# Optimization experiments

Measured on AMD Instinct MI355X. Metric: run time of the kernel, lower is better.

Reference implementation:

```python
import jax, jax.numpy as jnp
import numpy as np

CAPACITY = 1024


def setup_inputs() -> dict:
    T, H, I, E, K = 2048, 1024, 1408, 8, 2
    key = jax.random.key(0)
    k0, k1, k2, k3, k4 = jax.random.split(key, 5)
    hidden_states = jax.random.normal(k0, (T, H), dtype=jnp.float32)
    w1 = jax.random.normal(k1, (E, 2 * I, H), dtype=jnp.float32) * 0.02  # [gate; up]
    w2 = jax.random.normal(k2, (E, H, I), dtype=jnp.float32) * 0.02
    topk_weights = jax.random.uniform(k3, (T, K), dtype=jnp.float32)
    topk_ids = jax.random.randint(k4, (T, K), 0, E, dtype=jnp.int32)
    return {"hidden_states": hidden_states, "w1": w1, "w2": w2,
            "topk_weights": topk_weights, "topk_ids": topk_ids}


def reference(hidden_states, w1, w2, topk_weights, topk_ids):
    # MoE: prepare(dispatch) -> grouped expert GEMM (silu-gated MLP) -> finalize(combine)
    T, H = hidden_states.shape
    E = w1.shape[0]
    I = w2.shape[2]
    K = topk_ids.shape[1]
    C = CAPACITY

    # ---- prepare: dispatch token copies to per-expert buffers ----
    flat_ids = topk_ids.reshape(-1)                       # (T*K,)
    onehot = jax.nn.one_hot(flat_ids, E, dtype=jnp.int32)  # (T*K, E)
    cs = jnp.cumsum(onehot, axis=0)                        # running per-expert counts
    pos = jnp.take_along_axis(cs, flat_ids[:, None], axis=1)[:, 0] - 1  # slot in expert buffer
    keep = pos < C
    pos_c = jnp.where(keep, pos, 0)

    x_flat = jnp.repeat(hidden_states, K, axis=0)          # (T*K, H)
    x_e = jnp.zeros((E, C, H), dtype=hidden_states.dtype)
    x_e = x_e.at[flat_ids, pos_c].add(jnp.where(keep[:, None], x_flat, 0.0))

    # ---- grouped expert GEMM: silu(gate) * up, then down-proj ----
    h = jnp.einsum('ech,eoh->eco', x_e, w1)                # (E, C, 2I)
    gate, up = h[..., :I], h[..., I:]
    act = jax.nn.silu(gate) * up                           # (E, C, I)
    y = jnp.einsum('eci,ehi->ech', act, w2)                # (E, C, H)

    # ---- finalize: gather back, apply router weights, reduce over top-k ----
    y_flat = y[flat_ids, pos_c] * (keep[:, None].astype(y.dtype)) \
             * topk_weights.reshape(-1, 1)                 # (T*K, H)
    out = y_flat.reshape(T, K, H).sum(axis=1)              # (T, H)
    return out.astype(hidden_states.dtype)
```

## Files before the change

kernel.cpp:

```cpp
#include <hip/hip_runtime.h>

#define NE 8
#define CAP 1024
#define HD 1024
#define ID 1408
#define TT 2048

typedef __attribute__((ext_vector_type(8))) short bf16x8;
typedef __attribute__((ext_vector_type(4))) float f32x4;
typedef unsigned short u16;
typedef unsigned int u32;
typedef unsigned long long u64;

__device__ __forceinline__ u16 f2bf(float f) {
  u32 u = __float_as_uint(f);
  u = (u + 0x7fffu + ((u >> 16) & 1u)) >> 16;
  return (u16)u;
}

__device__ __forceinline__ void async_cp16(const void* g, void* l) {
  __builtin_amdgcn_global_load_lds(
      (const __attribute__((address_space(1))) u32*)g,
      (__attribute__((address_space(3))) u32*)l, 16, 0, 0);
}

#define W1_BLKS (2 * ID * NE)
#define W2_BLKS (NE * HD * ID / 4 / 256)
#define X_BLKS (TT * HD / 4 / 256)
__global__ void prep_kernel(const float4* __restrict__ w1, ushort4* __restrict__ bw1,
                            const float4* __restrict__ w2, ushort4* __restrict__ bw2,
                            const float4* __restrict__ x, ushort4* __restrict__ bx,
                            float4* __restrict__ out) {
  int b = blockIdx.x;
  int tid = threadIdx.x;
  if (b < W1_BLKS) {
    int n = b % (2 * ID);
    int e = b / (2 * ID);
    int j = (n < ID) ? n : (n - ID);
    int np = (j >> 4) * 32 + (j & 15) + ((n < ID) ? 0 : 16);
    float4 v = w1[((size_t)e * 2 * ID + n) * (HD / 4) + tid];
    ushort4 o;
    o.x = f2bf(v.x); o.y = f2bf(v.y); o.z = f2bf(v.z); o.w = f2bf(v.w);
    bw1[((size_t)e * 2 * ID + np) * (HD / 4) + tid] = o;
  } else if (b < W1_BLKS + W2_BLKS) {
    size_t i = (size_t)(b - W1_BLKS) * 256 + tid;
    float4 v = w2[i];
    ushort4 o;
    o.x = f2bf(v.x); o.y = f2bf(v.y); o.z = f2bf(v.z); o.w = f2bf(v.w);
    bw2[i] = o;
  } else {
    size_t i = (size_t)(b - W1_BLKS - W2_BLKS) * 256 + tid;
    float4 v = x[i];
    ushort4 o;
    o.x = f2bf(v.x); o.y = f2bf(v.y); o.z = f2bf(v.z); o.w = f2bf(v.w);
    bx[i] = o;
    out[i] = float4{0.f, 0.f, 0.f, 0.f};
  }
}

__global__ void route_kernel(const int* __restrict__ ids, int* __restrict__ rowmap,
                             int* __restrict__ flatpos, int* __restrict__ counts) {
  __shared__ int ids_s[TT * 2];
  __shared__ int sc[256][NE + 1];
  int tid = threadIdx.x;
  for (int i = tid; i < TT * 2; i += 256) ids_s[i] = ids[i];
  __syncthreads();
  int base = tid * 16;
  u64 own64 = 0;
#pragma unroll
  for (int j = 0; j < 16; ++j) own64 += 1ull << (ids_s[base + j] * 8);
  int own[NE];
#pragma unroll
  for (int e = 0; e < NE; ++e) { own[e] = (int)((own64 >> (e * 8)) & 0xff); sc[tid][e] = own[e]; }
  __syncthreads();
  for (int off = 1; off < 256; off <<= 1) {
    int v[NE];
    if (tid >= off) {
#pragma unroll
      for (int e = 0; e < NE; ++e) v[e] = sc[tid - off][e];
    }
    __syncthreads();
    if (tid >= off) {
#pragma unroll
      for (int e = 0; e < NE; ++e) sc[tid][e] += v[e];
    }
    __syncthreads();
  }
  if (tid == 255) {
#pragma unroll
    for (int e = 0; e < NE; ++e) counts[e] = sc[255][e] < CAP ? sc[255][e] : CAP;
  }
  int excl[NE];
#pragma unroll
  for (int e = 0; e < NE; ++e) excl[e] = sc[tid][e] - own[e];
  __syncthreads();
#pragma unroll
  for (int e = 0; e < NE; ++e) sc[tid][e] = excl[e];
#pragma unroll
  for (int j = 0; j < 16; ++j) {
    int f = base + j;
    int e = ids_s[f];
    int p = sc[tid][e]++;
    if (p < CAP) { rowmap[e * CAP + p] = f; flatpos[f] = p; }
    else flatpos[f] = -1;
  }
}

__global__ __launch_bounds__(256) void gemm1_kernel(
    const u16* __restrict__ A, const u16* __restrict__ B, u16* __restrict__ Hb,
    const int* __restrict__ rowmap, const int* __restrict__ counts) {
  int e = blockIdx.x;
  int count = counts[e];
  int m0 = blockIdx.y * 64;
  if (m0 >= count) return;
  int n0 = blockIdx.z * 128;
  int tid = threadIdx.x;
  int lane = tid & 63, wid = tid >> 6;
  int wm = wid >> 1, wn = wid & 1;
  int q = lane >> 4, lm = lane & 15;

  __shared__ __align__(16) char smA[64 * 128];
  __shared__ __align__(16) char smB[128 * 128];

  int rloc = tid >> 3;
  int chs = ((tid & 7) ^ (rloc & 7)) * 8;
  const u16* aP[2];
  const u16* bP[4];
#pragma unroll
  for (int i = 0; i < 2; ++i) {
    int gr = m0 + rloc + 32 * i;
    int f = (gr < count) ? rowmap[e * CAP + gr] : 0;
    aP[i] = A + (size_t)(f >> 1) * HD + chs;
  }
#pragma unroll
  for (int i = 0; i < 4; ++i)
    bP[i] = B + ((size_t)e * 2 * ID + n0 + rloc + 32 * i) * HD + chs;

  f32x4 zero = {0.f, 0.f, 0.f, 0.f};
  f32x4 acc[2][4];
#pragma unroll
  for (int mi = 0; mi < 2; ++mi)
#pragma unroll
    for (int ni = 0; ni < 4; ++ni) acc[mi][ni] = zero;

  for (int kt = 0; kt < HD / 64; ++kt) {
    int ko = kt * 64;
#pragma unroll
    for (int i = 0; i < 2; ++i)
      async_cp16(aP[i] + ko, smA + (i * 256 + tid) * 16);
#pragma unroll
    for (int i = 0; i < 4; ++i)
      async_cp16(bP[i] + ko, smB + (i * 256 + tid) * 16);
    asm volatile("s_waitcnt vmcnt(0)" ::: "memory");
    __syncthreads();
#pragma unroll
    for (int s = 0; s < 2; ++s) {
      bf16x8 af[2], bfr[4];
#pragma unroll
      for (int mi = 0; mi < 2; ++mi) {
        int row = wm * 32 + mi * 16 + lm;
        af[mi] = *(const bf16x8*)(smA + row * 128 + (((s * 4 + q) ^ (lm & 7)) * 16));
      }
#pragma unroll
      for (int ni = 0; ni < 4; ++ni) {
        int row = wn * 64 + ni * 16 + lm;
        bfr[ni] = *(const bf16x8*)(smB + row * 128 + (((s * 4 + q) ^ (lm & 7)) * 16));
      }
#pragma unroll
      for (int mi = 0; mi < 2; ++mi)
#pragma unroll
        for (int ni = 0; ni < 4; ++ni)
          acc[mi][ni] = __builtin_amdgcn_mfma_f32_16x16x32_bf16(af[mi], bfr[ni], acc[mi][ni], 0, 0, 0);
    }
    __syncthreads();
  }

  u16* smOut = (u16*)smB;
#pragma unroll
  for (int mi = 0; mi < 2; ++mi) {
#pragma unroll
    for (int k = 0; k < 2; ++k) {
      int colL = wn * 32 + k * 16 + lm;
#pragma unroll
      for (int r = 0; r < 4; ++r) {
        float g = acc[mi][2 * k][r];
        float u = acc[mi][2 * k + 1][r];
        float a = g / (1.f + __expf(-g)) * u;
        int row = wm * 32 + mi * 16 + q * 4 + r;
        smOut[row * 72 + colL] = f2bf(a);
      }
    }
  }
  __syncthreads();
  {
    int row = tid >> 2, seg = tid & 3;
    const u16* sp = smOut + row * 72 + seg * 16;
    bf16x8 v0 = *(const bf16x8*)sp;
    bf16x8 v1 = *(const bf16x8*)(sp + 8);
    u16* dp = Hb + ((size_t)e * CAP + m0 + row) * ID + (n0 >> 1) + seg * 16;
    *(bf16x8*)dp = v0;
    *(bf16x8*)(dp + 8) = v1;
  }
}

__global__ __launch_bounds__(256) void gemm2_kernel(
    const u16* __restrict__ A, const u16* __restrict__ B, float* __restrict__ out,
    const int* __restrict__ rowmap, const int* __restrict__ counts,
    const float* __restrict__ tw) {
  int e = blockIdx.x;
  int count = counts[e];
  int m0 = blockIdx.y * 64;
  if (m0 >= count) return;
  int n0 = blockIdx.z * 64;
  int tid = threadIdx.x;
  int lane = tid & 63, wid = tid >> 6;
  int wm = wid >> 1, wn = wid & 1;
  int q = lane >> 4, lm = lane & 15;

  __shared__ __align__(16) char smA[64 * 128];
  __shared__ __align__(16) char smB[64 * 128];

  int rloc = tid >> 3;
  int chs = ((tid & 7) ^ (rloc & 7)) * 8;
  const u16* aP[2];
  const u16* bP[2];
#pragma unroll
  for (int i = 0; i < 2; ++i) {
    aP[i] = A + ((size_t)e * CAP + m0 + rloc + 32 * i) * ID + chs;
    bP[i] = B + ((size_t)e * HD + n0 + rloc + 32 * i) * ID + chs;
  }

  f32x4 zero = {0.f, 0.f, 0.f, 0.f};
  f32x4 acc[2][2];
#pragma unroll
  for (int mi = 0; mi < 2; ++mi)
#pragma unroll
    for (int ni = 0; ni < 2; ++ni) acc[mi][ni] = zero;

  for (int kt = 0; kt < ID / 64; ++kt) {
    int ko = kt * 64;
#pragma unroll
    for (int i = 0; i < 2; ++i) {
      async_cp16(aP[i] + ko, smA + (i * 256 + tid) * 16);
      async_cp16(bP[i] + ko, smB + (i * 256 + tid) * 16);
    }
    asm volatile("s_waitcnt vmcnt(0)" ::: "memory");
    __syncthreads();
#pragma unroll
    for (int s = 0; s < 2; ++s) {
      bf16x8 af[2], bfr[2];
#pragma unroll
      for (int mi = 0; mi < 2; ++mi) {
        int row = wm * 32 + mi * 16 + lm;
        af[mi] = *(const bf16x8*)(smA + row * 128 + (((s * 4 + q) ^ (lm & 7)) * 16));
      }
#pragma unroll
      for (int ni = 0; ni < 2; ++ni) {
        int row = wn * 32 + ni * 16 + lm;
        bfr[ni] = *(const bf16x8*)(smB + row * 128 + (((s * 4 + q) ^ (lm & 7)) * 16));
      }
#pragma unroll
      for (int mi = 0; mi < 2; ++mi)
#pragma unroll
        for (int ni = 0; ni < 2; ++ni)
          acc[mi][ni] = __builtin_amdgcn_mfma_f32_16x16x32_bf16(af[mi], bfr[ni], acc[mi][ni], 0, 0, 0);
    }
    __syncthreads();
  }

#pragma unroll
  for (int mi = 0; mi < 2; ++mi) {
#pragma unroll
    for (int r = 0; r < 4; ++r) {
      int grow = m0 + wm * 32 + mi * 16 + q * 4 + r;
      if (grow < count) {
        int f = rowmap[e * CAP + grow];
        float w = tw[f];
        int t = f >> 1;
#pragma unroll
        for (int ni = 0; ni < 2; ++ni) {
          int col = n0 + wn * 32 + ni * 16 + lm;
          atomicAdd(&out[(size_t)t * HD + col], w * acc[mi][ni][r]);
        }
      }
    }
  }
}

extern "C" void kernel_launch(void* const* d_in, const int* in_sizes, int n_in,
                              void* d_out, int out_size, void* d_ws, size_t ws_size,
                              hipStream_t stream) {
  const float* hidden = (const float*)d_in[0];
  const float* w1 = (const float*)d_in[1];
  const float* w2 = (const float*)d_in[2];
  const float* tw = (const float*)d_in[3];
  const int* ids = (const int*)d_in[4];
  float* out = (float*)d_out;

  char* p = (char*)d_ws;
  auto alloc = [&](size_t b) { char* r = p; p += (b + 255) & ~(size_t)255; return r; };
  u16* bw1 = (u16*)alloc((size_t)NE * 2 * ID * HD * 2);
  u16* bw2 = (u16*)alloc((size_t)NE * HD * ID * 2);
  u16* bx = (u16*)alloc((size_t)TT * HD * 2);
  u16* hbuf = (u16*)alloc((size_t)NE * CAP * ID * 2);
  int* rowmap = (int*)alloc((size_t)NE * CAP * 4);
  int* flatpos = (int*)alloc((size_t)TT * 2 * 4);
  int* counts = (int*)alloc((size_t)NE * 4);

  prep_kernel<<<W1_BLKS + W2_BLKS + X_BLKS, 256, 0, stream>>>(
      (const float4*)w1, (ushort4*)bw1, (const float4*)w2, (ushort4*)bw2,
      (const float4*)hidden, (ushort4*)bx, (float4*)out);

  route_kernel<<<1, 256, 0, stream>>>(ids, rowmap, flatpos, counts);

  gemm1_kernel<<<dim3(NE, CAP / 64, 2 * ID / 128), 256, 0, stream>>>(
      bx, bw1, hbuf, rowmap, counts);

  gemm2_kernel<<<dim3(NE, CAP / 64, HD / 64), 256, 0, stream>>>(
      hbuf, bw2, out, rowmap, counts, tw);
}
```

Measured before the change: 265.9 us.

## Fuse fp32-to-bf16 conversion into GEMM loads with register double buffering

Removes the separate prep kernel that converted weights and activations to bf16 in workspace. The GEMM kernels now load fp32 directly into registers, convert them with packed bf16 instructions, and write to double-buffered LDS, with the next tile's loads overlapped with the current MFMA work. Routing and output zeroing are merged into one launch, and s_setprio is raised around the MFMA blocks. Each weight element is now re-read as fp32 by every M-tile block instead of once, which doubles the global bytes fetched per tile and adds conversion work inside the hot loop.

```diff
diff --git a/kernel.cpp b/kernel.cpp
--- a/kernel.cpp
+++ b/kernel.cpp
@@ -8,6 +8,7 @@
 
 typedef __attribute__((ext_vector_type(8))) short bf16x8;
 typedef __attribute__((ext_vector_type(4))) float f32x4;
+typedef __attribute__((ext_vector_type(4))) unsigned int u32x4;
 typedef unsigned short u16;
 typedef unsigned int u32;
 typedef unsigned long long u64;
@@ -18,96 +19,84 @@
   return (u16)u;
 }
 
-__device__ __forceinline__ void async_cp16(const void* g, void* l) {
-  __builtin_amdgcn_global_load_lds(
-      (const __attribute__((address_space(1))) u32*)g,
-      (__attribute__((address_space(3))) u32*)l, 16, 0, 0);
-}
-
-#define W1_BLKS (2 * ID * NE)
-#define W2_BLKS (NE * HD * ID / 4 / 256)
-#define X_BLKS (TT * HD / 4 / 256)
-__global__ void prep_kernel(const float4* __restrict__ w1, ushort4* __restrict__ bw1,
-                            const float4* __restrict__ w2, ushort4* __restrict__ bw2,
-                            const float4* __restrict__ x, ushort4* __restrict__ bx,
-                            float4* __restrict__ out) {
+__device__ __forceinline__ u32 pk2(float a, float b) {
+  u32 r;
+  asm("v_cvt_pk_bf16_f32 %0, %1, %2" : "=v"(r) : "v"(a), "v"(b));
+  return r;
+}
+__device__ __forceinline__ u32x4 cvt16(float4 a, float4 b) {
+  u32x4 w;
+  w.x = pk2(a.x, a.y);
+  w.y = pk2(a.z, a.w);
+  w.z = pk2(b.x, b.y);
+  w.w = pk2(b.z, b.w);
+  return w;
+}
+
+__global__ __launch_bounds__(256) void route_zero(
+    const int* __restrict__ ids, int* __restrict__ rowmap,
+    int* __restrict__ counts, float4* __restrict__ out) {
   int b = blockIdx.x;
   int tid = threadIdx.x;
-  if (b < W1_BLKS) {
-    int n = b % (2 * ID);
-    int e = b / (2 * ID);
-    int j = (n < ID) ? n : (n - ID);
-    int np = (j >> 4) * 32 + (j & 15) + ((n < ID) ? 0 : 16);
-    float4 v = w1[((size_t)e * 2 * ID + n) * (HD / 4) + tid];
-    ushort4 o;
-    o.x = f2bf(v.x); o.y = f2bf(v.y); o.z = f2bf(v.z); o.w = f2bf(v.w);
-    bw1[((size_t)e * 2 * ID + np) * (HD / 4) + tid] = o;
-  } else if (b < W1_BLKS + W2_BLKS) {
-    size_t i = (size_t)(b - W1_BLKS) * 256 + tid;
-    float4 v = w2[i];
-    ushort4 o;
-    o.x = f2bf(v.x); o.y = f2bf(v.y); o.z = f2bf(v.z); o.w = f2bf(v.w);
-    bw2[i] = o;
-  } else {
-    size_t i = (size_t)(b - W1_BLKS - W2_BLKS) * 256 + tid;
-    float4 v = x[i];
-    ushort4 o;
-    o.x = f2bf(v.x); o.y = f2bf(v.y); o.z = f2bf(v.z); o.w = f2bf(v.w);
-    bx[i] = o;
-    out[i] = float4{0.f, 0.f, 0.f, 0.f};
-  }
-}
-
-__global__ void route_kernel(const int* __restrict__ ids, int* __restrict__ rowmap,
-                             int* __restrict__ flatpos, int* __restrict__ counts) {
-  __shared__ int ids_s[TT * 2];
-  __shared__ int sc[256][NE + 1];
-  int tid = threadIdx.x;
-  for (int i = tid; i < TT * 2; i += 256) ids_s[i] = ids[i];
-  __syncthreads();
-  int base = tid * 16;
-  u64 own64 = 0;
-#pragma unroll
-  for (int j = 0; j < 16; ++j) own64 += 1ull << (ids_s[base + j] * 8);
-  int own[NE];
-#pragma unroll
-  for (int e = 0; e < NE; ++e) { own[e] = (int)((own64 >> (e * 8)) & 0xff); sc[tid][e] = own[e]; }
-  __syncthreads();
-  for (int off = 1; off < 256; off <<= 1) {
-    int v[NE];
-    if (tid >= off) {
-#pragma unroll
-      for (int e = 0; e < NE; ++e) v[e] = sc[tid - off][e];
-    }
-    __syncthreads();
-    if (tid >= off) {
-#pragma unroll
-      for (int e = 0; e < NE; ++e) sc[tid][e] += v[e];
-    }
-    __syncthreads();
-  }
-  if (tid == 255) {
-#pragma unroll
-    for (int e = 0; e < NE; ++e) counts[e] = sc[255][e] < CAP ? sc[255][e] : CAP;
-  }
-  int excl[NE];
-#pragma unroll
-  for (int e = 0; e < NE; ++e) excl[e] = sc[tid][e] - own[e];
-  __syncthreads();
-#pragma unroll
-  for (int e = 0; e < NE; ++e) sc[tid][e] = excl[e];
-#pragma unroll
-  for (int j = 0; j < 16; ++j) {
-    int f = base + j;
-    int e = ids_s[f];
-    int p = sc[tid][e]++;
-    if (p < CAP) { rowmap[e * CAP + p] = f; flatpos[f] = p; }
-    else flatpos[f] = -1;
-  }
-}
-
+  if (b == 0) {
+    __shared__ unsigned char ids_s[TT * 2];
+    __shared__ int sc[256][NE + 1];
+    for (int i = tid; i < TT * 2; i += 256) ids_s[i] = (unsigned char)ids[i];
+    __syncthreads();
+    int base = tid * 16;
+    u64 own64 = 0;
+#pragma unroll
+    for (int j = 0; j < 16; ++j) own64 += 1ull << (ids_s[base + j] * 8);
+    int own[NE];
+#pragma unroll
+    for (int e = 0; e < NE; ++e) {
+      own[e] = (int)((own64 >> (e * 8)) & 0xff);
+      sc[tid][e] = own[e];
+    }
+    __syncthreads();
+    for (int off = 1; off < 256; off <<= 1) {
+      int v[NE];
+      if (tid >= off) {
+#pragma unroll
+        for (int e = 0; e < NE; ++e) v[e] = sc[tid - off][e];
+      }
+      __syncthreads();
+      if (tid >= off) {
+#pragma unroll
+        for (int e = 0; e < NE; ++e) sc[tid][e] += v[e];
+      }
+      __syncthreads();
+    }
+    if (tid == 255) {
+#pragma unroll
+      for (int e = 0; e < NE; ++e) counts[e] = sc[255][e] < CAP ? sc[255][e] : CAP;
+    }
+    int excl[NE];
+#pragma unroll
+    for (int e = 0; e < NE; ++e) excl[e] = sc[tid][e] - own[e];
+    __syncthreads();
+#pragma unroll
+    for (int e = 0; e < NE; ++e) sc[tid][e] = excl[e];
+#pragma unroll
+    for (int j = 0; j < 16; ++j) {
+      int f = base + j;
+      int e = ids_s[f];
+      int p = sc[tid][e]++;
+      if (p < CAP) rowmap[e * CAP + p] = f;
+    }
+    return;
+  }
+  size_t i = (size_t)(b - 1) * 1024 + tid;
+  float4 z = {0.f, 0.f, 0.f, 0.f};
+  out[i] = z;
+  out[i + 256] = z;
+  out[i + 512] = z;
+  out[i + 768] = z;
+}
+
+#define G1BUF 24576
 __global__ __launch_bounds__(256) void gemm1_kernel(
-    const u16* __restrict__ A, const u16* __restrict__ B, u16* __restrict__ Hb,
+    const float4* __restrict__ X, const float4* __restrict__ W1, u16* __restrict__ Hb,
     const int* __restrict__ rowmap, const int* __restrict__ counts) {
   int e = blockIdx.x;
   int count = counts[e];
@@ -119,22 +108,26 @@
   int wm = wid >> 1, wn = wid & 1;
   int q = lane >> 4, lm = lane & 15;
 
-  __shared__ __align__(16) char smA[64 * 128];
-  __shared__ __align__(16) char smB[128 * 128];
+  __shared__ __align__(16) char sm[2 * G1BUF];
 
   int rloc = tid >> 3;
-  int chs = ((tid & 7) ^ (rloc & 7)) * 8;
-  const u16* aP[2];
-  const u16* bP[4];
+  int ch = (tid & 7) ^ (rloc & 7);
+
+  const float4* aQ[2];
 #pragma unroll
   for (int i = 0; i < 2; ++i) {
     int gr = m0 + rloc + 32 * i;
     int f = (gr < count) ? rowmap[e * CAP + gr] : 0;
-    aP[i] = A + (size_t)(f >> 1) * HD + chs;
-  }
-#pragma unroll
-  for (int i = 0; i < 4; ++i)
-    bP[i] = B + ((size_t)e * 2 * ID + n0 + rloc + 32 * i) * HD + chs;
+    aQ[i] = X + (size_t)(f >> 1) * (HD / 4) + ch * 2;
+  }
+  const float4* bQ[4];
+#pragma unroll
+  for (int i = 0; i < 4; ++i) {
+    int np = n0 + rloc + 32 * i;
+    int g = np >> 5, w = np & 31;
+    int n = (w < 16) ? (g * 16 + w) : (ID + g * 16 + (w - 16));
+    bQ[i] = W1 + ((size_t)e * 2 * ID + n) * (HD / 4) + ch * 2;
+  }
 
   f32x4 zero = {0.f, 0.f, 0.f, 0.f};
   f32x4 acc[2][4];
@@ -143,39 +136,58 @@
 #pragma unroll
     for (int ni = 0; ni < 4; ++ni) acc[mi][ni] = zero;
 
+  float4 a0, a1, a2, a3, b0, b1, b2, b3, b4, b5, b6, b7;
+#define LOAD1(kt)                                                       \
+  do {                                                                  \
+    int o_ = (kt) * 16;                                                 \
+    a0 = aQ[0][o_]; a1 = aQ[0][o_ + 1];                                 \
+    a2 = aQ[1][o_]; a3 = aQ[1][o_ + 1];                                 \
+    b0 = bQ[0][o_]; b1 = bQ[0][o_ + 1];                                 \
+    b2 = bQ[1][o_]; b3 = bQ[1][o_ + 1];                                 \
+    b4 = bQ[2][o_]; b5 = bQ[2][o_ + 1];                                 \
+    b6 = bQ[3][o_]; b7 = bQ[3][o_ + 1];                                 \
+  } while (0)
+#define CVTW1(base)                                                     \
+  do {                                                                  \
+    char* sb_ = (base);                                                 \
+    *(u32x4*)(sb_ + tid * 16) = cvt16(a0, a1);                          \
+    *(u32x4*)(sb_ + 4096 + tid * 16) = cvt16(a2, a3);                   \
+    *(u32x4*)(sb_ + 8192 + tid * 16) = cvt16(b0, b1);                   \
+    *(u32x4*)(sb_ + 12288 + tid * 16) = cvt16(b2, b3);                  \
+    *(u32x4*)(sb_ + 16384 + tid * 16) = cvt16(b4, b5);                  \
+    *(u32x4*)(sb_ + 20480 + tid * 16) = cvt16(b6, b7);                  \
+  } while (0)
+
+  LOAD1(0);
+  CVTW1(sm);
+  __syncthreads();
   for (int kt = 0; kt < HD / 64; ++kt) {
-    int ko = kt * 64;
-#pragma unroll
-    for (int i = 0; i < 2; ++i)
-      async_cp16(aP[i] + ko, smA + (i * 256 + tid) * 16);
-#pragma unroll
-    for (int i = 0; i < 4; ++i)
-      async_cp16(bP[i] + ko, smB + (i * 256 + tid) * 16);
-    asm volatile("s_waitcnt vmcnt(0)" ::: "memory");
-    __syncthreads();
+    char* cb = sm + (kt & 1) * G1BUF;
+    char* nb = sm + ((kt & 1) ^ 1) * G1BUF;
+    if (kt < HD / 64 - 1) LOAD1(kt + 1);
 #pragma unroll
     for (int s = 0; s < 2; ++s) {
+      int cs = ((s * 4 + q) ^ (lm & 7)) * 16;
       bf16x8 af[2], bfr[4];
 #pragma unroll
-      for (int mi = 0; mi < 2; ++mi) {
-        int row = wm * 32 + mi * 16 + lm;
-        af[mi] = *(const bf16x8*)(smA + row * 128 + (((s * 4 + q) ^ (lm & 7)) * 16));
-      }
-#pragma unroll
-      for (int ni = 0; ni < 4; ++ni) {
-        int row = wn * 64 + ni * 16 + lm;
-        bfr[ni] = *(const bf16x8*)(smB + row * 128 + (((s * 4 + q) ^ (lm & 7)) * 16));
-      }
+      for (int mi = 0; mi < 2; ++mi)
+        af[mi] = *(const bf16x8*)(cb + (wm * 32 + mi * 16 + lm) * 128 + cs);
+#pragma unroll
+      for (int ni = 0; ni < 4; ++ni)
+        bfr[ni] = *(const bf16x8*)(cb + 8192 + (wn * 64 + ni * 16 + lm) * 128 + cs);
+      __builtin_amdgcn_s_setprio(1);
 #pragma unroll
       for (int mi = 0; mi < 2; ++mi)
 #pragma unroll
         for (int ni = 0; ni < 4; ++ni)
           acc[mi][ni] = __builtin_amdgcn_mfma_f32_16x16x32_bf16(af[mi], bfr[ni], acc[mi][ni], 0, 0, 0);
-    }
-    __syncthreads();
-  }
-
-  u16* smOut = (u16*)smB;
+      __builtin_amdgcn_s_setprio(0);
+    }
+    if (kt < HD / 64 - 1) CVTW1(nb);
+    __syncthreads();
+  }
+
+  u16* smOut = (u16*)sm;
 #pragma unroll
   for (int mi = 0; mi < 2; ++mi) {
 #pragma unroll
@@ -203,8 +215,9 @@
   }
 }
 
+#define G2BUF 16384
 __global__ __launch_bounds__(256) void gemm2_kernel(
-    const u16* __restrict__ A, const u16* __restrict__ B, float* __restrict__ out,
+    const u16* __restrict__ A, const float4* __restrict__ W2, float* __restrict__ out,
     const int* __restrict__ rowmap, const int* __restrict__ counts,
     const float* __restrict__ tw) {
   int e = blockIdx.x;
@@ -217,18 +230,19 @@
   int wm = wid >> 1, wn = wid & 1;
   int q = lane >> 4, lm = lane & 15;
 
-  __shared__ __align__(16) char smA[64 * 128];
-  __shared__ __align__(16) char smB[64 * 128];
+  __shared__ __align__(16) char sm[2 * G2BUF];
 
   int rloc = tid >> 3;
-  int chs = ((tid & 7) ^ (rloc & 7)) * 8;
-  const u16* aP[2];
-  const u16* bP[2];
-#pragma unroll
-  for (int i = 0; i < 2; ++i) {
-    aP[i] = A + ((size_t)e * CAP + m0 + rloc + 32 * i) * ID + chs;
-    bP[i] = B + ((size_t)e * HD + n0 + rloc + 32 * i) * ID + chs;
-  }
+  int ch = (tid & 7) ^ (rloc & 7);
+
+  const u32x4* aU[2];
+#pragma unroll
+  for (int i = 0; i < 2; ++i)
+    aU[i] = (const u32x4*)A + (size_t)(e * CAP + m0 + rloc + 32 * i) * (ID / 8) + ch;
+  const float4* bQ[2];
+#pragma unroll
+  for (int i = 0; i < 2; ++i)
+    bQ[i] = W2 + ((size_t)e * HD + n0 + rloc + 32 * i) * (ID / 4) + ch * 2;
 
   f32x4 zero = {0.f, 0.f, 0.f, 0.f};
   f32x4 acc[2][2];
@@ -237,34 +251,49 @@
 #pragma unroll
     for (int ni = 0; ni < 2; ++ni) acc[mi][ni] = zero;
 
+  u32x4 A0, A1;
+  float4 c0, c1, c2, c3;
+#define LOAD2(kt)                                                       \
+  do {                                                                  \
+    A0 = aU[0][(kt) * 8]; A1 = aU[1][(kt) * 8];                         \
+    c0 = bQ[0][(kt) * 16]; c1 = bQ[0][(kt) * 16 + 1];                   \
+    c2 = bQ[1][(kt) * 16]; c3 = bQ[1][(kt) * 16 + 1];                   \
+  } while (0)
+#define CVTW2(base)                                                     \
+  do {                                                                  \
+    char* sb_ = (base);                                                 \
+    *(u32x4*)(sb_ + tid * 16) = A0;                                     \
+    *(u32x4*)(sb_ + 4096 + tid * 16) = A1;                              \
+    *(u32x4*)(sb_ + 8192 + tid * 16) = cvt16(c0, c1);                   \
+    *(u32x4*)(sb_ + 12288 + tid * 16) = cvt16(c2, c3);                  \
+  } while (0)
+
+  LOAD2(0);
+  CVTW2(sm);
+  __syncthreads();
   for (int kt = 0; kt < ID / 64; ++kt) {
-    int ko = kt * 64;
-#pragma unroll
-    for (int i = 0; i < 2; ++i) {
-      async_cp16(aP[i] + ko, smA + (i * 256 + tid) * 16);
-      async_cp16(bP[i] + ko, smB + (i * 256 + tid) * 16);
-    }
-    asm volatile("s_waitcnt vmcnt(0)" ::: "memory");
-    __syncthreads();
+    char* cb = sm + (kt & 1) * G2BUF;
+    char* nb = sm + ((kt & 1) ^ 1) * G2BUF;
+    if (kt < ID / 64 - 1) LOAD2(kt + 1);
 #pragma unroll
     for (int s = 0; s < 2; ++s) {
+      int cs = ((s * 4 + q) ^ (lm & 7)) * 16;
       bf16x8 af[2], bfr[2];
 #pragma unroll
-      for (int mi = 0; mi < 2; ++mi) {
-        int row = wm * 32 + mi * 16 + lm;
-        af[mi] = *(const bf16x8*)(smA + row * 128 + (((s * 4 + q) ^ (lm & 7)) * 16));
-      }
-#pragma unroll
-      for (int ni = 0; ni < 2; ++ni) {
-        int row = wn * 32 + ni * 16 + lm;
-        bfr[ni] = *(const bf16x8*)(smB + row * 128 + (((s * 4 + q) ^ (lm & 7)) * 16));
-      }
+      for (int mi = 0; mi < 2; ++mi)
+        af[mi] = *(const bf16x8*)(cb + (wm * 32 + mi * 16 + lm) * 128 + cs);
+#pragma unroll
+      for (int ni = 0; ni < 2; ++ni)
+        bfr[ni] = *(const bf16x8*)(cb + 8192 + (wn * 32 + ni * 16 + lm) * 128 + cs);
+      __builtin_amdgcn_s_setprio(1);
 #pragma unroll
       for (int mi = 0; mi < 2; ++mi)
 #pragma unroll
         for (int ni = 0; ni < 2; ++ni)
           acc[mi][ni] = __builtin_amdgcn_mfma_f32_16x16x32_bf16(af[mi], bfr[ni], acc[mi][ni], 0, 0, 0);
-    }
+      __builtin_amdgcn_s_setprio(0);
+    }
+    if (kt < ID / 64 - 1) CVTW2(nb);
     __syncthreads();
   }
 
@@ -299,23 +328,15 @@
 
   char* p = (char*)d_ws;
   auto alloc = [&](size_t b) { char* r = p; p += (b + 255) & ~(size_t)255; return r; };
-  u16* bw1 = (u16*)alloc((size_t)NE * 2 * ID * HD * 2);
-  u16* bw2 = (u16*)alloc((size_t)NE * HD * ID * 2);
-  u16* bx = (u16*)alloc((size_t)TT * HD * 2);
   u16* hbuf = (u16*)alloc((size_t)NE * CAP * ID * 2);
   int* rowmap = (int*)alloc((size_t)NE * CAP * 4);
-  int* flatpos = (int*)alloc((size_t)TT * 2 * 4);
   int* counts = (int*)alloc((size_t)NE * 4);
 
-  prep_kernel<<<W1_BLKS + W2_BLKS + X_BLKS, 256, 0, stream>>>(
-      (const float4*)w1, (ushort4*)bw1, (const float4*)w2, (ushort4*)bw2,
-      (const float4*)hidden, (ushort4*)bx, (float4*)out);
-
-  route_kernel<<<1, 256, 0, stream>>>(ids, rowmap, flatpos, counts);
+  route_zero<<<513, 256, 0, stream>>>(ids, rowmap, counts, (float4*)out);
 
   gemm1_kernel<<<dim3(NE, CAP / 64, 2 * ID / 128), 256, 0, stream>>>(
-      bx, bw1, hbuf, rowmap, counts);
+      (const float4*)hidden, (const float4*)w1, hbuf, rowmap, counts);
 
   gemm2_kernel<<<dim3(NE, CAP / 64, HD / 64), 256, 0, stream>>>(
-      hbuf, bw2, out, rowmap, counts, tw);
-}
+      hbuf, (const float4*)w2, out, rowmap, counts, tw);
+}
```

Result: slower. 304.5 us (+14.5%).
